# Kernel optimization log

Hardware: AMD Instinct MI355X
Metric: run time of the kernel (lower is better)

Reference implementation:

```python
import jax, jax.numpy as jnp
import numpy as np

NEG_SLOPE = 0.2  # GAT LeakyReLU slope
EPS = 1e-16


def _pagat_conv(x, path_index, W, a, b, heads, out_ch, concat):
    """Path-augmented GAT conv: attention over (head, mid, tail) path triples,
    messages flow tail -> head, softmax-normalized per destination node."""
    N = x.shape[0]
    head, mid, tail = path_index[0], path_index[1], path_index[2]
    h = (x @ W).reshape(N, heads, out_ch)            # [N, H, C]
    # attention logits from all three path positions: [P, H]
    e = (jnp.einsum('phc,hc->ph', h[head], a[0])
         + jnp.einsum('phc,hc->ph', h[mid], a[1])
         + jnp.einsum('phc,hc->ph', h[tail], a[2]))
    e = jax.nn.leaky_relu(e, NEG_SLOPE)
    # segment softmax over paths grouped by destination (head) node
    m = jax.ops.segment_max(e, head, num_segments=N)  # [N, H]
    ex = jnp.exp(e - m[head])
    s = jax.ops.segment_sum(ex, head, num_segments=N)  # [N, H]
    alpha = ex / (s[head] + EPS)                       # [P, H]
    # aggregate tail features weighted by attention
    out = jax.ops.segment_sum(alpha[..., None] * h[tail], head, num_segments=N)  # [N, H, C]
    if concat:
        out = out.reshape(N, heads * out_ch)
    else:
        out = out.mean(axis=1)
    return out + b


def setup_inputs() -> dict:
    key = jax.random.key(0)
    ks = jax.random.split(key, 8)
    N, F_in, H, C, CLS, P = 100000, 500, 8, 16, 16, 1000000
    x = jax.random.normal(ks[0], (N, F_in), dtype=jnp.float32)
    path_index = jax.random.randint(ks[1], (3, P), 0, N, dtype=jnp.int32)
    W1 = jax.random.normal(ks[2], (F_in, H * C), dtype=jnp.float32) * 0.05
    a1 = jax.random.normal(ks[3], (3, H, C), dtype=jnp.float32) * 0.05
    b1 = jnp.zeros((H * C,), dtype=jnp.float32)
    W2 = jax.random.normal(ks[4], (H * C, CLS), dtype=jnp.float32) * 0.05
    a2 = jax.random.normal(ks[5], (3, 1, CLS), dtype=jnp.float32) * 0.05
    b2 = jnp.zeros((CLS,), dtype=jnp.float32)
    return {"x": x, "path_index": path_index, "W1": W1, "a1": a1, "b1": b1,
            "W2": W2, "a2": a2, "b2": b2}


def reference(x, path_index, W1, a1, b1, W2, a2, b2):
    # eval mode: dropout is identity
    h = _pagat_conv(x, path_index, W1, a1, b1, heads=8, out_ch=16, concat=True)
    h = jax.nn.elu(h)
    h = _pagat_conv(h, path_index, W2, a2, b2, heads=1, out_ch=16, concat=False)
    return jax.nn.log_softmax(h, axis=1)
```

## Files before the change

kernel.cpp:

```cpp
#include <hip/hip_runtime.h>
#include <hip/hip_bf16.h>

#define F_IN  500
#define HC    128
#define NHEAD 8
#define CDIM  16
#define NCLS  16
#define KPAD  512

static __device__ __forceinline__ float bf(const __hip_bfloat16 v) {
    return __bfloat162float(v);
}

static __device__ __forceinline__ unsigned int enc_f32(float f) {
    unsigned int u = __float_as_uint(f);
    return (u & 0x80000000u) ? ~u : (u | 0x80000000u);
}
static __device__ __forceinline__ float dec_f32(unsigned int u) {
    return __uint_as_float((u & 0x80000000u) ? (u & 0x7FFFFFFFu) : ~u);
}

typedef __bf16 bf16x8 __attribute__((ext_vector_type(8)));
typedef float f32x4 __attribute__((ext_vector_type(4)));

static __device__ __forceinline__ void gload16(const void* g, void* l) {
    __builtin_amdgcn_global_load_lds(
        (const __attribute__((address_space(1))) void*)g,
        (__attribute__((address_space(3))) void*)l, 16, 0, 0);
}

static __device__ __forceinline__ unsigned ldsoff(const void* p) {
    return (unsigned)(size_t)(const __attribute__((address_space(3))) void*)p;
}

static __device__ __forceinline__ void ds_read_f4(unsigned addr, float4& out) {
    asm volatile("ds_read_b128 %0, %1" : "=v"(out) : "v"(addr) : "memory");
}

template<int OFF>
static __device__ __forceinline__ bf16x8 gld_b(const __bf16* p) {
    bf16x8 o;
    asm volatile("global_load_dwordx4 %0, %1, off offset:%2"
                 : "=v"(o) : "v"(p), "i"(OFF) : "memory");
    return o;
}

__global__ void prep_kernel(const float* __restrict__ W1,
                            __bf16* __restrict__ w1t_hi,
                            __bf16* __restrict__ w1t_lo,
                            int* __restrict__ zp, int nz)
{
    int e = blockIdx.x * 256 + threadIdx.x;
    if (e < HC * KPAD) {
        int j = e & 7, lane = (e >> 3) & 63, ct = (e >> 9) & 3;
        int t = (e >> 11) & 15, wc = (e >> 15) & 1;
        int c = wc * 64 + ct * 16 + (lane & 15);
        int k = t * 32 + (lane >> 4) * 8 + j;
        float v = (k < F_IN) ? W1[k * HC + c] : 0.f;
        __bf16 h = (__bf16)v;
        w1t_hi[e] = h;
        w1t_lo[e] = (__bf16)(v - (float)h);
    }
    if (e < nz) zp[e] = 0;
}

static __device__ __forceinline__ void split8(const float4 a, const float4 b,
                                              bf16x8& hi, bf16x8& lo) {
    float v[8] = {a.x, a.y, a.z, a.w, b.x, b.y, b.z, b.w};
#pragma unroll
    for (int j = 0; j < 8; j++) {
        __bf16 h = (__bf16)v[j];
        hi[j] = h;
        lo[j] = (__bf16)(v[j] - (float)h);
    }
}

__global__ __launch_bounds__(256, 3) void gemm1_v8(
    const float* __restrict__ x,
    const __bf16* __restrict__ w1hi, const __bf16* __restrict__ w1lo,
    const float* __restrict__ zpad,
    __hip_bfloat16* __restrict__ h1,
    const float* __restrict__ a1, float* __restrict__ d1,
    unsigned int* __restrict__ gmax,
    const int* __restrict__ pidx, int* __restrict__ deg, int N, int P)
{
    __shared__ float As[4][64 * 32];
    __shared__ unsigned int smax[16];

    const int tid = threadIdx.x;
    const int lane = tid & 63, wave = tid >> 6;
    const int m = lane & 15, q = lane >> 4;
    const int wr = wave >> 1, wc = wave & 1;
    const int n0 = blockIdx.x * 64;
    const int woff = wave << 10;

    if (tid < 16) smax[tid] = 0;

    auto stage = [&](int buf, int t) {
        const int k0 = t * 32;
#pragma unroll
        for (int j = 0; j < 2; ++j) {
            int idx = j * 256 + tid;
            int r = idx >> 3, ps = idx & 7;
            int ls = ps ^ (r & 7);
            int kk = k0 + ls * 4;
            int grow = n0 + r;
            const float* src = (kk < F_IN)
                ? (x + (size_t)(grow < N ? grow : 0) * F_IN + kk)
                : zpad;
            gload16(src, (char*)&As[buf][0] + j * 4096 + woff);
        }
    };

    const __bf16* bh_base = w1hi + (size_t)wc * 32768 + (size_t)lane * 8;
    const __bf16* bl_base = w1lo + (size_t)wc * 32768 + (size_t)lane * 8;

    auto loadB = [&](bf16x8 (&bh)[4], bf16x8 (&bl)[4], int t) {
        const __bf16* ph = bh_base + (size_t)t * 2048;
        const __bf16* pl = bl_base + (size_t)t * 2048;
        bh[0] = gld_b<0>(ph);    bh[1] = gld_b<1024>(ph);
        bh[2] = gld_b<2048>(ph); bh[3] = gld_b<3072>(ph);
        bl[0] = gld_b<0>(pl);    bl[1] = gld_b<1024>(pl);
        bl[2] = gld_b<2048>(pl); bl[3] = gld_b<3072>(pl);
    };

    unsigned abase[4];
#pragma unroll
    for (int i = 0; i < 4; ++i) abase[i] = ldsoff(&As[i][0]);
    unsigned aoffs[2][2];
#pragma unroll
    for (int rt = 0; rt < 2; ++rt) {
        int r = wr * 32 + rt * 16 + m, x7 = r & 7;
        aoffs[rt][0] = r * 128 + (((2 * q) ^ x7) << 4);
        aoffs[rt][1] = r * 128 + (((2 * q + 1) ^ x7) << 4);
    }

    f32x4 acc[2][4];
#pragma unroll
    for (int rt = 0; rt < 2; ++rt)
#pragma unroll
        for (int ct = 0; ct < 4; ++ct) acc[rt][ct] = (f32x4){0.f, 0.f, 0.f, 0.f};

    bf16x8 bhA[4], blA[4], bhB[4], blB[4];

    stage(0, 0);
    stage(1, 1);
    loadB(bhA, blA, 0);
    stage(2, 2);

    auto compute = [&](bf16x8 (&bh)[4], bf16x8 (&bl)[4],
                       bf16x8 (&ah)[2], bf16x8 (&al)[2]) {
        __builtin_amdgcn_s_setprio(1);
#pragma unroll
        for (int rt = 0; rt < 2; ++rt)
#pragma unroll
            for (int ct = 0; ct < 4; ++ct) {
                acc[rt][ct] = __builtin_amdgcn_mfma_f32_16x16x32_bf16(ah[rt], bh[ct], acc[rt][ct], 0, 0, 0);
                acc[rt][ct] = __builtin_amdgcn_mfma_f32_16x16x32_bf16(ah[rt], bl[ct], acc[rt][ct], 0, 0, 0);
                acc[rt][ct] = __builtin_amdgcn_mfma_f32_16x16x32_bf16(al[rt], bh[ct], acc[rt][ct], 0, 0, 0);
            }
        __builtin_amdgcn_s_setprio(0);
    };

#pragma unroll
    for (int t = 0; t < 16; ++t) {
        if (t > 0) __builtin_amdgcn_s_barrier();
        if (t + 1 < 16) {
            if ((t & 1) == 0) loadB(bhB, blB, t + 1);
            else              loadB(bhA, blA, t + 1);
        }
        if (t + 3 < 16) stage((t + 3) & 3, t + 3);

        if (t <= 12)      asm volatile("s_waitcnt vmcnt(12)" ::: "memory");
        else if (t == 13) asm volatile("s_waitcnt vmcnt(10)" ::: "memory");
        else if (t == 14) asm volatile("s_waitcnt vmcnt(8)" ::: "memory");
        else              asm volatile("s_waitcnt vmcnt(0)" ::: "memory");
        __builtin_amdgcn_s_barrier();

        const int cur = t & 3;
        float4 fa[2][2];
        ds_read_f4(abase[cur] + aoffs[0][0], fa[0][0]);
        ds_read_f4(abase[cur] + aoffs[0][1], fa[0][1]);
        ds_read_f4(abase[cur] + aoffs[1][0], fa[1][0]);
        ds_read_f4(abase[cur] + aoffs[1][1], fa[1][1]);
        asm volatile("s_waitcnt lgkmcnt(0)" ::: "memory");
        __builtin_amdgcn_sched_barrier(0);

        bf16x8 ah[2], al[2];
        split8(fa[0][0], fa[0][1], ah[0], al[0]);
        split8(fa[1][0], fa[1][1], ah[1], al[1]);

        if ((t & 1) == 0) compute(bhA, blA, ah, al);
        else              compute(bhB, blB, ah, al);
    }

#pragma unroll
    for (int rt = 0; rt < 2; ++rt) {
        int rbase = n0 + wr * 32 + rt * 16 + q * 4;
#pragma unroll
        for (int ct = 0; ct < 4; ++ct) {
            int col = wc * 64 + ct * 16 + m;
#pragma unroll
            for (int r = 0; r < 4; ++r) {
                int row = rbase + r;
                if (row < N)
                    h1[(size_t)row * HC + col] = __float2bfloat16(acc[rt][ct][r]);
            }
        }
    }

#pragma unroll
    for (int rt = 0; rt < 2; ++rt)
#pragma unroll
        for (int ct = 0; ct < 4; ++ct) {
            int h = wc * 4 + ct;
            float w0 = a1[(0 * NHEAD + h) * CDIM + m];
            float w1 = a1[(1 * NHEAD + h) * CDIM + m];
            float w2 = a1[(2 * NHEAD + h) * CDIM + m];
#pragma unroll
            for (int r = 0; r < 4; ++r) {
                float v = bf(__float2bfloat16(acc[rt][ct][r]));
                float s0 = v * w0, s1 = v * w1, s2 = v * w2;
#pragma unroll
                for (int w = 1; w < 16; w <<= 1) {
                    s0 += __shfl_xor(s0, w, 16);
                    s1 += __shfl_xor(s1, w, 16);
                    s2 += __shfl_xor(s2, w, 16);
                }
                int row = n0 + wr * 32 + rt * 16 + q * 4 + r;
                if (m == 0 && row < N) {
                    d1[(size_t)row * NHEAD + h] = s0;
                    d1[(size_t)N * NHEAD + (size_t)row * NHEAD + h] = s1;
                    d1[(size_t)2 * N * NHEAD + (size_t)row * NHEAD + h] = s2;
                    atomicMax(&smax[h], enc_f32(s1));
                    atomicMax(&smax[8 + h], enc_f32(s2));
                }
            }
        }
    __syncthreads();
    if (tid < 16) atomicMax(&gmax[tid], smax[tid]);

    const int gsz = gridDim.x * 256;
    for (int i = blockIdx.x * 256 + tid; i < P; i += gsz)
        atomicAdd(deg + pidx[i], 1);
}

__global__ void scan1_kernel(const int* __restrict__ deg, int* __restrict__ start,
                             int* __restrict__ bsum, int N) {
    __shared__ int sh[256];
    int i = blockIdx.x * 256 + threadIdx.x;
    int v = (i < N) ? deg[i] : 0;
    sh[threadIdx.x] = v;
    __syncthreads();
#pragma unroll
    for (int off = 1; off < 256; off <<= 1) {
        int x = (threadIdx.x >= off) ? sh[threadIdx.x - off] : 0;
        __syncthreads();
        sh[threadIdx.x] += x;
        __syncthreads();
    }
    if (i < N) start[i] = sh[threadIdx.x] - v;
    if (threadIdx.x == 255) bsum[blockIdx.x] = sh[255];
}

__global__ void scan2_kernel(int* __restrict__ bsum, int nb) {
    __shared__ int sh[512];
    int v = (threadIdx.x < nb) ? bsum[threadIdx.x] : 0;
    sh[threadIdx.x] = v;
    __syncthreads();
#pragma unroll
    for (int off = 1; off < 512; off <<= 1) {
        int x = (threadIdx.x >= off) ? sh[threadIdx.x - off] : 0;
        __syncthreads();
        sh[threadIdx.x] += x;
        __syncthreads();
    }
    if (threadIdx.x < nb) bsum[threadIdx.x] = sh[threadIdx.x] - v;
}

__global__ void scan3_kernel(int* __restrict__ start, const int* __restrict__ bsum, int N) {
    int i = blockIdx.x * 256 + threadIdx.x;
    if (i < N) start[i] += bsum[blockIdx.x];
}

__global__ void scatter_kernel(const int* __restrict__ pidx,
                               const int* __restrict__ start,
                               int* __restrict__ cursor,
                               int* __restrict__ csr, int P) {
    int p = blockIdx.x * blockDim.x + threadIdx.x;
    if (p >= P) return;
    int hd = pidx[p];
    int pos = atomicAdd(cursor + hd, 1);
    csr[start[hd] + pos] = p;
}

__global__ __launch_bounds__(256) void attn1_csr_kernel(
    const int* __restrict__ csr, const int* __restrict__ start,
    const int* __restrict__ deg, const int* __restrict__ pidx,
    const float* __restrict__ d1, const __hip_bfloat16* __restrict__ h1,
    const float* __restrict__ b1, const unsigned int* __restrict__ gmax,
    float* __restrict__ elu_out, int N, int P)
{
    int node = blockIdx.x * 4 + (threadIdx.x >> 6);
    if (node >= N) return;
    int lane = threadIdx.x & 63;
    int h = lane >> 3;
    int s0 = start[node], dg = deg[node];
    const float* d1m = d1 + (size_t)N * NHEAD;
    const float* d1t = d1 + (size_t)2 * N * NHEAD;
    const float dh = d1[node * NHEAD + h];
    float zub = dh + dec_f32(gmax[h]) + dec_f32(gmax[8 + h]);
    const float mxub = zub > 0.f ? zub : 0.2f * zub;

    float acc0 = 0.f, acc1 = 0.f, den = 0.f;
    for (int k0 = 0; k0 < dg; k0 += 8) {
        int kk = k0 + (lane & 7);
        bool valid = kk < dg;
        int p = csr[s0 + (valid ? kk : dg - 1)];
        int mid = pidx[P + p], tl = pidx[2 * P + p];
        float z = dh + d1m[mid * NHEAD + h] + d1t[tl * NHEAD + h];
        float e = z > 0.f ? z : 0.2f * z;
        float ex = valid ? __expf(e - mxub) : 0.f;
        den += ex;
        __hip_bfloat162 v[8];
        float exs[8];
#pragma unroll
        for (int dk = 0; dk < 8; dk++) {
            int tl_b = __shfl(tl, dk, 8);
            exs[dk] = __shfl(ex, dk, 8);
            v[dk] = *(const __hip_bfloat162*)(h1 + (size_t)tl_b * HC + 2 * lane);
        }
#pragma unroll
        for (int dk = 0; dk < 8; dk++) {
            acc0 += exs[dk] * bf(v[dk].x);
            acc1 += exs[dk] * bf(v[dk].y);
        }
    }
#pragma unroll
    for (int w = 1; w < 8; w <<= 1) den += __shfl_xor(den, w, 8);

    float inv = 1.f / (den + 1e-16f);
    int j0 = 2 * lane;
    float v0 = acc0 * inv + b1[j0];
    float v1 = acc1 * inv + b1[j0 + 1];
    v0 = v0 > 0.f ? v0 : __expf(v0) - 1.f;
    v1 = v1 > 0.f ? v1 : __expf(v1) - 1.f;
    *(float2*)(elu_out + (size_t)node * HC + j0) = make_float2(v0, v1);
}

__global__ __launch_bounds__(256) void layer2_kernel(
    const float* __restrict__ elu, const float* __restrict__ W2,
    const float* __restrict__ a2,
    float* __restrict__ h2, float* __restrict__ d2,
    unsigned int* __restrict__ gmax2, int N)
{
    __shared__ float rows[64][HC + 4];
    __shared__ float h2s[64][NCLS + 1];
    __shared__ unsigned int smax[2];
    const int n0 = blockIdx.x * 64;
    const int tid = threadIdx.x;
    if (tid < 2) smax[tid] = 0;
    for (int idx = tid; idx < 64 * 32; idx += 256) {
        int r = idx >> 5, c4 = idx & 31;
        float4 v = (n0 + r < N)
            ? *(const float4*)&elu[(size_t)(n0 + r) * HC + c4 * 4]
            : make_float4(0.f, 0.f, 0.f, 0.f);
        *(float4*)&rows[r][c4 * 4] = v;
    }
    __syncthreads();
    int ln = tid >> 4, c = tid & 15;
#pragma unroll
    for (int pass = 0; pass < 4; ++pass) {
        int r = pass * 16 + ln;
        float acc = 0.f;
#pragma unroll 8
        for (int j = 0; j < HC; j++) acc += rows[r][j] * W2[j * NCLS + c];
        h2s[r][c] = acc;
        if (n0 + r < N) h2[(size_t)(n0 + r) * NCLS + c] = acc;
    }
    __syncthreads();
    if (tid < 192) {
        int l = tid / 3, j = tid - l * 3;
        if (n0 + l < N) {
            float s = 0.f;
#pragma unroll
            for (int cc = 0; cc < NCLS; cc++) s += h2s[l][cc] * a2[j * NCLS + cc];
            d2[j * N + n0 + l] = s;
            if (j) atomicMax(&smax[j - 1], enc_f32(s));
        }
    }
    __syncthreads();
    if (tid < 2) atomicMax(&gmax2[tid], smax[tid]);
}

__global__ __launch_bounds__(256) void attn2_csr_kernel(
    const int* __restrict__ csr, const int* __restrict__ start,
    const int* __restrict__ deg, const int* __restrict__ pidx,
    const float* __restrict__ d2, const float* __restrict__ h2,
    const float* __restrict__ b2, const unsigned int* __restrict__ gmax2,
    float* __restrict__ out, int N, int P)
{
    int node = blockIdx.x * 16 + (threadIdx.x >> 4);
    if (node >= N) return;
    int c = threadIdx.x & 15;
    int s0 = start[node], dg = deg[node];
    const float dh = d2[node];
    const float* d2m = d2 + N;
    const float* d2t = d2 + 2 * N;
    float zub = dh + dec_f32(gmax2[0]) + dec_f32(gmax2[1]);
    const float mxub = zub > 0.f ? zub : 0.2f * zub;

    float acc = 0.f, den = 0.f;
    for (int k0 = 0; k0 < dg; k0 += 16) {
        int kk = k0 + c;
        bool valid = kk < dg;
        int p = csr[s0 + (valid ? kk : dg - 1)];
        int mid = pidx[P + p], tl = pidx[2 * P + p];
        float z = dh + d2m[mid] + d2t[tl];
        float e = z > 0.f ? z : 0.2f * z;
        float ex = valid ? __expf(e - mxub) : 0.f;
        den += ex;
        float vv[16], exs[16];
#pragma unroll
        for (int dk = 0; dk < 16; dk++) {
            int tl_b = __shfl(tl, dk, 16);
            exs[dk] = __shfl(ex, dk, 16);
            vv[dk] = h2[(size_t)tl_b * NCLS + c];
        }
#pragma unroll
        for (int dk = 0; dk < 16; dk++) acc += exs[dk] * vv[dk];
    }
#pragma unroll
    for (int w = 1; w < 16; w <<= 1) den += __shfl_xor(den, w, 16);

    float o = acc / (den + 1e-16f) + b2[c];
    float m2 = o;
#pragma unroll
    for (int w = 1; w < 16; w <<= 1) m2 = fmaxf(m2, __shfl_xor(m2, w, 16));
    float ex = __expf(o - m2), sm = ex;
#pragma unroll
    for (int w = 1; w < 16; w <<= 1) sm += __shfl_xor(sm, w, 16);
    float r = o - m2 - __logf(sm);
    out[(size_t)node * NCLS + c] = r;
}

extern "C" void kernel_launch(void* const* d_in, const int* in_sizes, int n_in,
                              void* d_out, int out_size, void* d_ws, size_t ws_size,
                              hipStream_t stream)
{
    const float* x  = (const float*)d_in[0];
    const int*   pi = (const int*)d_in[1];
    const float* W1 = (const float*)d_in[2];
    const float* a1 = (const float*)d_in[3];
    const float* b1 = (const float*)d_in[4];
    const float* W2 = (const float*)d_in[5];
    const float* a2 = (const float*)d_in[6];
    const float* b2 = (const float*)d_in[7];

    const int N = in_sizes[0] / F_IN;
    const int P = in_sizes[1] / 3;

    float* ws = (float*)d_ws;
    size_t off_h1     = 0;
    size_t off_d1     = (size_t)64 * N;
    size_t off_elu    = (size_t)88 * N;
    size_t off_h2     = (size_t)216 * N;
    size_t off_d2     = (size_t)232 * N;
    size_t off_deg    = (size_t)235 * N;
    size_t off_start  = (size_t)236 * N;
    size_t off_cursor = (size_t)237 * N;
    size_t off_gmax   = (size_t)238 * N;
    size_t off_zpad   = (size_t)238 * N + 32;
    size_t off_bsum   = (size_t)238 * N + 96;
    size_t off_csr    = (size_t)238 * N + 96 + 1024;
    size_t off_w1th   = off_csr + P;
    size_t off_w1tl   = off_w1th + 32768;

    __hip_bfloat16* h1 = (__hip_bfloat16*)(ws + off_h1);
    float* d1   = ws + off_d1;
    float* elu  = ws + off_elu;
    float* h2   = ws + off_h2;
    float* d2   = ws + off_d2;
    int* deg    = (int*)(ws + off_deg);
    int* start  = (int*)(ws + off_start);
    int* cursor = (int*)(ws + off_cursor);
    unsigned int* gmax  = (unsigned int*)(ws + off_gmax);
    unsigned int* gmax2 = (unsigned int*)(ws + off_gmax) + 16;
    float* zpad = ws + off_zpad;
    int* bsum   = (int*)(ws + off_bsum);
    int* csr    = (int*)(ws + off_csr);
    __bf16* w1t_hi = (__bf16*)(ws + off_w1th);
    __bf16* w1t_lo = (__bf16*)(ws + off_w1tl);

    const int BLK = 256;
    const int nb = (N + 255) / 256;
    const int nz = 3 * N + 96;
    const int nprep = (HC * KPAD > nz ? HC * KPAD : nz);

    prep_kernel<<<(nprep + 255) / 256, 256, 0, stream>>>(W1, w1t_hi, w1t_lo, deg, nz);
    gemm1_v8<<<(N + 63) / 64, 256, 0, stream>>>(x, w1t_hi, w1t_lo, zpad, h1,
                                                a1, d1, gmax, pi, deg, N, P);
    scan1_kernel<<<nb, 256, 0, stream>>>(deg, start, bsum, N);
    scan2_kernel<<<1, 512, 0, stream>>>(bsum, nb);
    scan3_kernel<<<nb, 256, 0, stream>>>(start, bsum, N);
    scatter_kernel<<<(P + BLK - 1) / BLK, BLK, 0, stream>>>(pi, start, cursor, csr, P);
    attn1_csr_kernel<<<(N + 3) / 4, 256, 0, stream>>>(csr, start, deg, pi, d1, h1, b1, gmax, elu, N, P);
    layer2_kernel<<<(N + 63) / 64, 256, 0, stream>>>(elu, W2, a2, h2, d2, gmax2, N);
    attn2_csr_kernel<<<(N + 15) / 16, 256, 0, stream>>>(csr, start, deg, pi, d2, h2, b2, gmax2,
                                                        (float*)d_out, N, P);
}
```

Before: 611.5 us.

## Fuse layer-2 projection and logit computation into layer-1 attention epilogue

After: 1.604 ms. 2.62x slower.

```diff
diff --git a/kernel.cpp b/kernel.cpp
--- a/kernel.cpp
+++ b/kernel.cpp
@@ -48,6 +48,8 @@
 __global__ void prep_kernel(const float* __restrict__ W1,
                             __bf16* __restrict__ w1t_hi,
                             __bf16* __restrict__ w1t_lo,
+                            const float* __restrict__ W2,
+                            float* __restrict__ w2t,
                             int* __restrict__ zp, int nz)
 {
     int e = blockIdx.x * 256 + threadIdx.x;
@@ -60,6 +62,10 @@
         __bf16 h = (__bf16)v;
         w1t_hi[e] = h;
         w1t_lo[e] = (__bf16)(v - (float)h);
+    }
+    if (e < NCLS * HC) {
+        int c = e >> 7, j = e & 127;
+        w2t[e] = W2[j * NCLS + c];
     }
     if (e < nz) zp[e] = 0;
 }
@@ -294,103 +300,102 @@
     csr[start[hd] + pos] = p;
 }
 
-__global__ __launch_bounds__(256) void attn1_csr_kernel(
+__global__ __launch_bounds__(256) void attn1_fused_kernel(
     const int* __restrict__ csr, const int* __restrict__ start,
     const int* __restrict__ deg, const int* __restrict__ pidx,
     const float* __restrict__ d1, const __hip_bfloat16* __restrict__ h1,
     const float* __restrict__ b1, const unsigned int* __restrict__ gmax,
-    float* __restrict__ elu_out, int N, int P)
+    const float* __restrict__ w2t, const float* __restrict__ a2,
+    float* __restrict__ h2, float* __restrict__ d2,
+    unsigned int* __restrict__ gmax2, int N, int P)
 {
-    int node = blockIdx.x * 4 + (threadIdx.x >> 6);
-    if (node >= N) return;
-    int lane = threadIdx.x & 63;
-    int h = lane >> 3;
-    int s0 = start[node], dg = deg[node];
-    const float* d1m = d1 + (size_t)N * NHEAD;
-    const float* d1t = d1 + (size_t)2 * N * NHEAD;
-    const float dh = d1[node * NHEAD + h];
-    float zub = dh + dec_f32(gmax[h]) + dec_f32(gmax[8 + h]);
-    const float mxub = zub > 0.f ? zub : 0.2f * zub;
-
-    float acc0 = 0.f, acc1 = 0.f, den = 0.f;
-    for (int k0 = 0; k0 < dg; k0 += 8) {
-        int kk = k0 + (lane & 7);
-        bool valid = kk < dg;
-        int p = csr[s0 + (valid ? kk : dg - 1)];
-        int mid = pidx[P + p], tl = pidx[2 * P + p];
-        float z = dh + d1m[mid * NHEAD + h] + d1t[tl * NHEAD + h];
-        float e = z > 0.f ? z : 0.2f * z;
-        float ex = valid ? __expf(e - mxub) : 0.f;
-        den += ex;
-        __hip_bfloat162 v[8];
-        float exs[8];
-#pragma unroll
-        for (int dk = 0; dk < 8; dk++) {
-            int tl_b = __shfl(tl, dk, 8);
-            exs[dk] = __shfl(ex, dk, 8);
-            v[dk] = *(const __hip_bfloat162*)(h1 + (size_t)tl_b * HC + 2 * lane);
-        }
-#pragma unroll
-        for (int dk = 0; dk < 8; dk++) {
-            acc0 += exs[dk] * bf(v[dk].x);
-            acc1 += exs[dk] * bf(v[dk].y);
-        }
-    }
-#pragma unroll
-    for (int w = 1; w < 8; w <<= 1) den += __shfl_xor(den, w, 8);
-
-    float inv = 1.f / (den + 1e-16f);
-    int j0 = 2 * lane;
-    float v0 = acc0 * inv + b1[j0];
-    float v1 = acc1 * inv + b1[j0 + 1];
-    v0 = v0 > 0.f ? v0 : __expf(v0) - 1.f;
-    v1 = v1 > 0.f ? v1 : __expf(v1) - 1.f;
-    *(float2*)(elu_out + (size_t)node * HC + j0) = make_float2(v0, v1);
-}
-
-__global__ __launch_bounds__(256) void layer2_kernel(
-    const float* __restrict__ elu, const float* __restrict__ W2,
-    const float* __restrict__ a2,
-    float* __restrict__ h2, float* __restrict__ d2,
-    unsigned int* __restrict__ gmax2, int N)
-{
-    __shared__ float rows[64][HC + 4];
-    __shared__ float h2s[64][NCLS + 1];
-    __shared__ unsigned int smax[2];
-    const int n0 = blockIdx.x * 64;
-    const int tid = threadIdx.x;
-    if (tid < 2) smax[tid] = 0;
-    for (int idx = tid; idx < 64 * 32; idx += 256) {
-        int r = idx >> 5, c4 = idx & 31;
-        float4 v = (n0 + r < N)
-            ? *(const float4*)&elu[(size_t)(n0 + r) * HC + c4 * 4]
-            : make_float4(0.f, 0.f, 0.f, 0.f);
-        *(float4*)&rows[r][c4 * 4] = v;
+    __shared__ float es[4][128];
+    __shared__ unsigned int smax2[2];
+
+    const int wv = threadIdx.x >> 6;
+    const int lane = threadIdx.x & 63;
+    const int node = blockIdx.x * 4 + wv;
+    const bool active = node < N;
+    if (threadIdx.x < 2) smax2[threadIdx.x] = 0;
+
+    if (active) {
+        int h = lane >> 3;
+        int s0 = start[node], dg = deg[node];
+        const float* d1m = d1 + (size_t)N * NHEAD;
+        const float* d1t = d1 + (size_t)2 * N * NHEAD;
+        const float dh = d1[node * NHEAD + h];
+        float zub = dh + dec_f32(gmax[h]) + dec_f32(gmax[8 + h]);
+        const float mxub = zub > 0.f ? zub : 0.2f * zub;
+
+        float acc0 = 0.f, acc1 = 0.f, den = 0.f;
+        for (int k0 = 0; k0 < dg; k0 += 8) {
+            int kk = k0 + (lane & 7);
+            bool valid = kk < dg;
+            int p = csr[s0 + (valid ? kk : dg - 1)];
+            int mid = pidx[P + p], tl = pidx[2 * P + p];
+            float z = dh + d1m[mid * NHEAD + h] + d1t[tl * NHEAD + h];
+            float e = z > 0.f ? z : 0.2f * z;
+            float ex = valid ? __expf(e - mxub) : 0.f;
+            den += ex;
+            __hip_bfloat162 v[8];
+            float exs[8];
+#pragma unroll
+            for (int dk = 0; dk < 8; dk++) {
+                int tl_b = __shfl(tl, dk, 8);
+                exs[dk] = __shfl(ex, dk, 8);
+                v[dk] = *(const __hip_bfloat162*)(h1 + (size_t)tl_b * HC + 2 * lane);
+            }
+#pragma unroll
+            for (int dk = 0; dk < 8; dk++) {
+                acc0 += exs[dk] * bf(v[dk].x);
+                acc1 += exs[dk] * bf(v[dk].y);
+            }
+        }
+#pragma unroll
+        for (int w = 1; w < 8; w <<= 1) den += __shfl_xor(den, w, 8);
+
+        float inv = 1.f / (den + 1e-16f);
+        int j0 = 2 * lane;
+        float v0 = acc0 * inv + b1[j0];
+        float v1 = acc1 * inv + b1[j0 + 1];
+        v0 = v0 > 0.f ? v0 : __expf(v0) - 1.f;
+        v1 = v1 > 0.f ? v1 : __expf(v1) - 1.f;
+        es[wv][j0] = v0;
+        es[wv][j0 + 1] = v1;
+
+        const int c = lane & 15, g = lane >> 4;
+        const float* ep = &es[wv][g * 32];
+        const float* wp = w2t + c * HC + g * 32;
+        float s = 0.f;
+#pragma unroll
+        for (int j4 = 0; j4 < 8; ++j4) {
+            float4 ev = *(const float4*)(ep + j4 * 4);
+            float4 wv4 = *(const float4*)(wp + j4 * 4);
+            s += ev.x * wv4.x + ev.y * wv4.y + ev.z * wv4.z + ev.w * wv4.w;
+        }
+        s += __shfl_xor(s, 16, 64);
+        s += __shfl_xor(s, 32, 64);
+        if (g == 0) h2[(size_t)node * NCLS + c] = s;
+
+        float t0 = s * a2[0 * NCLS + c];
+        float t1 = s * a2[1 * NCLS + c];
+        float t2 = s * a2[2 * NCLS + c];
+#pragma unroll
+        for (int w = 1; w < 16; w <<= 1) {
+            t0 += __shfl_xor(t0, w, 16);
+            t1 += __shfl_xor(t1, w, 16);
+            t2 += __shfl_xor(t2, w, 16);
+        }
+        if (lane == 0) {
+            d2[node] = t0;
+            d2[N + node] = t1;
+            d2[2 * N + node] = t2;
+            atomicMax(&smax2[0], enc_f32(t1));
+            atomicMax(&smax2[1], enc_f32(t2));
+        }
     }
     __syncthreads();
-    int ln = tid >> 4, c = tid & 15;
-#pragma unroll
-    for (int pass = 0; pass < 4; ++pass) {
-        int r = pass * 16 + ln;
-        float acc = 0.f;
-#pragma unroll 8
-        for (int j = 0; j < HC; j++) acc += rows[r][j] * W2[j * NCLS + c];
-        h2s[r][c] = acc;
-        if (n0 + r < N) h2[(size_t)(n0 + r) * NCLS + c] = acc;
-    }
-    __syncthreads();
-    if (tid < 192) {
-        int l = tid / 3, j = tid - l * 3;
-        if (n0 + l < N) {
-            float s = 0.f;
-#pragma unroll
-            for (int cc = 0; cc < NCLS; cc++) s += h2s[l][cc] * a2[j * NCLS + cc];
-            d2[j * N + n0 + l] = s;
-            if (j) atomicMax(&smax[j - 1], enc_f32(s));
-        }
-    }
-    __syncthreads();
-    if (tid < 2) atomicMax(&gmax2[tid], smax[tid]);
+    if (threadIdx.x < 2) atomicMax(&gmax2[threadIdx.x], smax2[threadIdx.x]);
 }
 
 __global__ __launch_bounds__(256) void attn2_csr_kernel(
@@ -463,7 +468,7 @@
     float* ws = (float*)d_ws;
     size_t off_h1     = 0;
     size_t off_d1     = (size_t)64 * N;
-    size_t off_elu    = (size_t)88 * N;
+    size_t off_w2t    = (size_t)88 * N;
     size_t off_h2     = (size_t)216 * N;
     size_t off_d2     = (size_t)232 * N;
     size_t off_deg    = (size_t)235 * N;
@@ -478,7 +483,7 @@
 
     __hip_bfloat16* h1 = (__hip_bfloat16*)(ws + off_h1);
     float* d1   = ws + off_d1;
-    float* elu  = ws + off_elu;
+    float* w2t  = ws + off_w2t;
     float* h2   = ws + off_h2;
     float* d2   = ws + off_d2;
     int* deg    = (int*)(ws + off_deg);
@@ -497,15 +502,15 @@
     const int nz = 3 * N + 96;
     const int nprep = (HC * KPAD > nz ? HC * KPAD : nz);
 
-    prep_kernel<<<(nprep + 255) / 256, 256, 0, stream>>>(W1, w1t_hi, w1t_lo, deg, nz);
+    prep_kernel<<<(nprep + 255) / 256, 256, 0, stream>>>(W1, w1t_hi, w1t_lo, W2, w2t, deg, nz);
     gemm1_v8<<<(N + 63) / 64, 256, 0, stream>>>(x, w1t_hi, w1t_lo, zpad, h1,
                                                 a1, d1, gmax, pi, deg, N, P);
     scan1_kernel<<<nb, 256, 0, stream>>>(deg, start, bsum, N);
     scan2_kernel<<<1, 512, 0, stream>>>(bsum, nb);
     scan3_kernel<<<nb, 256, 0, stream>>>(start, bsum, N);
     scatter_kernel<<<(P + BLK - 1) / BLK, BLK, 0, stream>>>(pi, start, cursor, csr, P);
-    attn1_csr_kernel<<<(N + 3) / 4, 256, 0, stream>>>(csr, start, deg, pi, d1, h1, b1, gmax, elu, N, P);
-    layer2_kernel<<<(N + 63) / 64, 256, 0, stream>>>(elu, W2, a2, h2, d2, gmax2, N);
+    attn1_fused_kernel<<<(N + 3) / 4, 256, 0, stream>>>(csr, start, deg, pi, d1, h1, b1, gmax,
+                                                        w2t, a2, h2, d2, gmax2, N, P);
     attn2_csr_kernel<<<(N + 15) / 16, 256, 0, stream>>>(csr, start, deg, pi, d2, h2, b2, gmax2,
                                                         (float*)d_out, N, P);
 }
```
